# Kernel tuning notes

Hardware: AMD Instinct MI355X
Metric: run time of the kernel (lower is better)

The kernel has to match this reference:

```python
import jax, jax.numpy as jnp
import numpy as np

EPS_NORM = 1e-5   # instance-norm epsilon (NormalizeLayer over spatial axes)
EPS_VAR = 1e-9    # floor used before sqrt, as in the original


def _instance_norm(x):
    # normalize over spatial axes (1,2), per batch & channel
    mean = jnp.mean(x, axis=(1, 2), keepdims=True)
    var = jnp.var(x, axis=(1, 2), keepdims=True)
    return (x - mean) * jax.lax.rsqrt(var + EPS_NORM)


def _aat(content, style, comb_c, comb_s):
    # content/style: (B,H,W,C); comb_*: (B,H,W,Cc)
    B, H, W, C = content.shape
    N = H * W
    norm_content = _instance_norm(content)
    q = _instance_norm(comb_c).reshape(B, N, -1)   # (B,N,Cc)
    k = _instance_norm(comb_s).reshape(B, N, -1)   # (B,N,Cc)
    v = style.reshape(B, N, C)                     # (B,N,C)
    scores = jnp.einsum('bnc,bmc->bnm', q, k)      # Q_T @ K
    A = jax.nn.softmax(scores, axis=-1)            # (B,N,N)
    M = jnp.einsum('bnm,bmc->bnc', A, v)           # weighted mean
    S2 = jnp.einsum('bnm,bmc->bnc', A, v * v) - M * M  # weighted variance
    S = jnp.sqrt(jnp.maximum(jax.nn.relu(S2), EPS_VAR))
    S = S.reshape(B, H, W, C)
    M = M.reshape(B, H, W, C)
    return S * norm_content + M


def _feature_loss(cs, c, s, cc, sc):
    aat = _aat(c, s, cc, sc)
    return jnp.mean(jnp.square(cs - aat))


def setup_inputs() -> dict:
    key = jax.random.key(0)
    shapes = {
        'cs2': (4, 64, 64, 256), 'c2': (4, 64, 64, 256), 's2': (4, 64, 64, 256),
        'cc2': (4, 64, 64, 448), 'sc2': (4, 64, 64, 448),
        'cs3': (4, 32, 32, 512), 'c3': (4, 32, 32, 512), 's3': (4, 32, 32, 512),
        'cc3': (4, 32, 32, 960), 'sc3': (4, 32, 32, 960),
        'cs4': (4, 16, 16, 512), 'c4': (4, 16, 16, 512), 's4': (4, 16, 16, 512),
        'cc4': (4, 16, 16, 1472), 'sc4': (4, 16, 16, 1472),
    }
    keys = jax.random.split(key, len(shapes))
    return {name: jax.random.normal(k, shp, dtype=jnp.float32)
            for k, (name, shp) in zip(keys, shapes.items())}


def reference(cs2, c2, s2, cc2, sc2, cs3, c3, s3, cc3, sc3, cs4, c4, s4, cc4, sc4):
    loss = _feature_loss(cs2, c2, s2, cc2, sc2)
    loss = loss + _feature_loss(cs3, c3, s3, cc3, sc3)
    loss = loss + _feature_loss(cs4, c4, s4, cc4, sc4)
    return loss
```

## Files before the change

kernel.cpp:

```cpp
#include <hip/hip_runtime.h>
#include <math.h>

#define EPS_NORM 1e-5f
#define EPS_VAR  1e-9f
#define LOG2E    1.4426950408889634f

typedef unsigned short ushort_t;
typedef __attribute__((ext_vector_type(4))) float f32x4;
typedef _Float16 half8 __attribute__((ext_vector_type(8)));

#define MFMAH(a, b, c) __builtin_amdgcn_mfma_f32_16x16x32_f16((a), (b), (c), 0, 0, 0)

#define GLD16(gp, lp) __builtin_amdgcn_global_load_lds(                          \
    (const __attribute__((address_space(1))) unsigned int*)(gp),                 \
    (__attribute__((address_space(3))) unsigned int*)(lp), 16, 0, 0)

__device__ inline ushort_t f16_bits(float x) {
    _Float16 h = (_Float16)x;
    ushort_t u;
    __builtin_memcpy(&u, &h, 2);
    return u;
}
__device__ inline half8 ldh(const ushort_t* p) {
    half8 h;
    __builtin_memcpy(&h, p, 16);
    return h;
}
__device__ inline uint4 pack8(const ushort_t* s) {
    uint4 r;
    r.x = (unsigned)s[0] | ((unsigned)s[1] << 16);
    r.y = (unsigned)s[2] | ((unsigned)s[3] << 16);
    r.z = (unsigned)s[4] | ((unsigned)s[5] << 16);
    r.w = (unsigned)s[6] | ((unsigned)s[7] << 16);
    return r;
}

struct StatJobs {
    const float* x[9];
    float* sm[9];
    float* sq[9];
    int N[9], Cn[9], chG[9], nG[9], base[9];
};
__global__ void __launch_bounds__(256) stat_partial_all(StatJobs J)
{
    int bx = blockIdx.x;
    int j = 0;
#pragma unroll
    for (int k = 1; k < 9; ++k) if (bx >= J.base[k]) j = k;
    bx -= J.base[j];
    const int N = J.N[j], Cn = J.Cn[j], chG = J.chG[j], nG = J.nG[j];
    int b  = bx / (chG * nG);
    int r  = bx % (chG * nG);
    int cg = r / nG;
    int ng = r % nG;
    int ch = cg * 256 + threadIdx.x;
    if (ch >= Cn) return;
    int n0 = ng * 256;
    int n1 = min(n0 + 256, N);
    const float* p = J.x[j] + (long)(b * N) * Cn + ch;
    float s = 0.f, ss = 0.f;
    for (int n = n0; n < n1; ++n) {
        float v = p[(long)n * Cn];
        s += v;
        ss = fmaf(v, v, ss);
    }
    atomicAdd(&J.sm[j][b * Cn + ch], s);
    atomicAdd(&J.sq[j][b * Cn + ch], ss);
}

struct FinJobs {
    float* sm[9];
    float* sq[9];
    int base[9];
    float invN[9];
    int total;
};
__global__ void __launch_bounds__(256) stat_finalize_all(FinJobs J)
{
    int i = blockIdx.x * 256 + threadIdx.x;
    if (i >= J.total) return;
    int j = 0;
#pragma unroll
    for (int k = 1; k < 9; ++k) if (i >= J.base[k]) j = k;
    int e = i - J.base[j];
    float m = J.sm[j][e] * J.invN[j];
    float v = J.sq[j][e] * J.invN[j] - m * m;
    J.sm[j][e] = m;
    J.sq[j][e] = rsqrtf(v + EPS_NORM);
}

struct PrepJobs {
    const float* qx[3]; const float* qm[3]; const float* qr[3]; ushort_t* qh[3];
    const float* kx[3]; const float* km[3]; const float* kr[3]; ushort_t* kh[3];
    const float* vx[3]; ushort_t* vt[3];
    int N[3], Cc[3], C[3], nbase[3];
};
__global__ void __launch_bounds__(256) prep_all(PrepJobs J)
{
    __shared__ __align__(16) ushort_t tbuf[64 * 72];
    int bx = blockIdx.x;
    int j = 0;
#pragma unroll
    for (int k = 1; k < 3; ++k) if (bx >= J.nbase[k]) j = k;
    bx -= J.nbase[j];
    const int N = J.N[j], Cc = J.Cc[j];
    const int normBlocks = 2 * N;
    if (bx < normBlocks) {
        const int wave = threadIdx.x >> 6, lane = threadIdx.x & 63;
        int rr = bx * 4 + wave;
        const int BN = 4 * N;
        const bool isQ = rr < BN;
        int bn = isQ ? rr : rr - BN;
        const float* x    = isQ ? J.qx[j] : J.kx[j];
        const float* mean = isQ ? J.qm[j] : J.km[j];
        const float* rstd = isQ ? J.qr[j] : J.kr[j];
        ushort_t* out     = isQ ? J.qh[j] : J.kh[j];
        const float scl   = isQ ? LOG2E : 1.0f;
        int b = bn / N;
        long base = (long)bn * Cc;
        const float* mb = mean + b * Cc;
        const float* rb = rstd + b * Cc;
        for (int c8 = lane; c8 * 8 < Cc; c8 += 64) {
            int ch = c8 * 8;
            float4 a0 = *(const float4*)(x + base + ch);
            float4 a1 = *(const float4*)(x + base + ch + 4);
            float4 m0 = *(const float4*)(mb + ch);
            float4 m1 = *(const float4*)(mb + ch + 4);
            float4 r0 = *(const float4*)(rb + ch);
            float4 r1 = *(const float4*)(rb + ch + 4);
            ushort_t h8[8];
            h8[0] = f16_bits((a0.x - m0.x) * r0.x * scl);
            h8[1] = f16_bits((a0.y - m0.y) * r0.y * scl);
            h8[2] = f16_bits((a0.z - m0.z) * r0.z * scl);
            h8[3] = f16_bits((a0.w - m0.w) * r0.w * scl);
            h8[4] = f16_bits((a1.x - m1.x) * r1.x * scl);
            h8[5] = f16_bits((a1.y - m1.y) * r1.y * scl);
            h8[6] = f16_bits((a1.z - m1.z) * r1.z * scl);
            h8[7] = f16_bits((a1.w - m1.w) * r1.w * scl);
            *(uint4*)(out + base + ch) = pack8(h8);
        }
    } else {
        int bid2 = bx - normBlocks;
        const int C = J.C[j];
        const int cT = C >> 6, nT = N >> 6;
        int b   = bid2 / (cT * nT);
        int rem = bid2 % (cT * nT);
        int ch0 = (rem / nT) << 6;
        int n0  = (rem % nT) << 6;
        const int lane = threadIdx.x & 63, wv = threadIdx.x >> 6;
        const float* vb_ = J.vx[j] + (long)b * N * C + ch0 + lane;
#pragma unroll
        for (int jj = 0; jj < 2; ++jj) {
            int nl = wv * 16 + jj * 8;
            ushort_t h8[8];
#pragma unroll
            for (int i = 0; i < 8; ++i)
                h8[i] = f16_bits(vb_[(long)(n0 + nl + i) * C]);
            *(uint4*)&tbuf[lane * 72 + nl] = pack8(h8);
        }
        __syncthreads();
        {
            const int chl = threadIdx.x >> 2;
            const int nq  = (threadIdx.x & 3) * 16;
            ushort_t* op = J.vt[j] + ((long)b * C + ch0 + chl) * N + n0 + nq;
            *(uint4*)op       = *(const uint4*)&tbuf[chl * 72 + nq];
            *(uint4*)(op + 8) = *(const uint4*)&tbuf[chl * 72 + nq + 8];
        }
    }
}

__device__ inline void stage64_async(const ushort_t* __restrict__ g, long rowBase,
                                     int gstride, int col0, ushort_t* slab, int tid)
{
    const int l  = tid & 63, w = tid >> 6;
    const int rs = l >> 3;
    const int cg = (l & 7) ^ rs;
#pragma unroll
    for (int i = 0; i < 2; ++i) {
        const int r = w * 16 + i * 8 + rs;
        const ushort_t* gp = g + (rowBase + r) * (long)gstride + col0 + (cg << 3);
        ushort_t* lp = slab + (w * 16 + i * 8) * 64 + l * 8;
        GLD16(gp, lp);
    }
}
template<int BROWS>
__device__ inline void stageQ_async(const ushort_t* __restrict__ g, long rowBase,
                                    int gstride, int col0, ushort_t* slab, int tid)
{
    if (tid < BROWS * 8) {
        const int l  = tid & 63, w = tid >> 6;
        const int rs = l >> 3;
        const int cg = (l & 7) ^ rs;
        const int r  = w * 8 + rs;
        const ushort_t* gp = g + (rowBase + r) * (long)gstride + col0 + (cg << 3);
        ushort_t* lp = slab + w * 8 * 64 + l * 8;
        GLD16(gp, lp);
    }
}
__device__ inline half8 ldsw(const ushort_t* slab, int row, int soff)
{
    const int gr = (soff >> 3) ^ (row & 7);
    return ldh(slab + row * 64 + (gr << 3));
}

__global__ void __launch_bounds__(256, 2) flash_pipe(
    const ushort_t* __restrict__ Qh, const ushort_t* __restrict__ Kh,
    const ushort_t* __restrict__ Vth,
    float* __restrict__ Pmo, float* __restrict__ Plo,
    float* __restrict__ PMo, float* __restrict__ PSo)
{
    constexpr int Cc = 448, C = 256, N = 4096, SPLIT = 2;
    constexpr int NKT  = (N / 64) / SPLIT;
    constexpr long VCHO = 64L * N;
    constexpr long KADV = 64L * Cc;

    __shared__ __align__(16) ushort_t smem[4 * 8192 + 4 * 1152];
    const int tid  = threadIdx.x;
    const int lane = tid & 63;
    const int w    = tid >> 6;
    const int l15  = lane & 15;
    const int quad = lane >> 4;
// ... 408 lines not shown
        half8 pf1 = ldh(Pw + l15 * 72 + 32 + quad * 8);

#pragma unroll
        for (int g = 0; g < VCW; g += G) {
            __syncthreads();
#pragma unroll
            for (int s = 0; s < 4; ++s) {
                const int h = s / G, j = s % G;
                stage64_async(Vth, (long)b * C + (h * VCW + g + j) * 64, N, kt * 64,
                              smem + s * 4096, tid);
            }
            __syncthreads();
#pragma unroll
            for (int ks = 0; ks < 2; ++ks) {
                half8 pf = ks ? pf1 : pf0;
#pragma unroll
                for (int j = 0; j < G; ++j)
#pragma unroll
                    for (int ct = 0; ct < 4; ++ct) {
                        half8 vh = ldsw(smem + (ch2 * G + j) * 4096,
                                        ct * 16 + l15, ks * 32 + quad * 8);
                        half8 uh = vh * vh;
                        const int ci = (g + j) * 4 + ct;
                        Mac[ci] = MFMAH(pf, vh, Mac[ci]);
                        Sac[ci] = MFMAH(pf, uh, Sac[ci]);
                    }
            }
        }
    }

#pragma unroll
    for (int off = 1; off <= 8; off <<= 1)
#pragma unroll
        for (int r = 0; r < 4; ++r) l_l[r] += __shfl_xor(l_l[r], off, 64);

    if (ch2 == 0 && l15 == 0) {
#pragma unroll
        for (int r = 0; r < 4; ++r) {
            Pmo[po * 16 + quad * 4 + r] = m_r[r];
            Plo[po * 16 + quad * 4 + r] = l_l[r];
        }
    }
    const int chb = ch2 * (C / CSPLIT);
#pragma unroll
    for (int ct = 0; ct < CTCW; ++ct)
#pragma unroll
        for (int r = 0; r < 4; ++r) {
            long idx = (po * 16 + quad * 4 + r) * C + chb + ct * 16 + l15;
            PMo[idx] = Mac[ct][r];
            PSo[idx] = Sac[ct][r];
        }
}

template<int Cc, int C, int N, int CSPLIT, bool QREG, int SPLIT, int SLABS, int KGRP>
__global__ void __launch_bounds__(256, 2) flash_mfma(
    const ushort_t* __restrict__ Qh, const ushort_t* __restrict__ Kh,
    const ushort_t* __restrict__ Vth,
    float* __restrict__ Pmo, float* __restrict__ Plo,
    float* __restrict__ PMo, float* __restrict__ PSo)
{
    __shared__ __align__(16) ushort_t smem[35328];
    flash_body<Cc, C, N, CSPLIT, QREG, SPLIT, SLABS, KGRP>(
        Qh, Kh, Vth, Pmo, Plo, PMo, PSo, smem, (int)blockIdx.x);
}

__global__ void __launch_bounds__(256, 2) flash34(
    const ushort_t* __restrict__ Qh3, const ushort_t* __restrict__ Kh3,
    const ushort_t* __restrict__ Vth3,
    float* __restrict__ Pm3, float* __restrict__ Pl3,
    float* __restrict__ PM3, float* __restrict__ PS3,
    const ushort_t* __restrict__ Qh4, const ushort_t* __restrict__ Kh4,
    const ushort_t* __restrict__ Vth4,
    float* __restrict__ Pm4, float* __restrict__ Pl4,
    float* __restrict__ PM4, float* __restrict__ PS4, int G3)
{
    __shared__ __align__(16) ushort_t smem[35328];
    if ((int)blockIdx.x < G3)
        flash_body<960, 512, 1024, 2, false, 4, 5, 5>(
            Qh3, Kh3, Vth3, Pm3, Pl3, PM3, PS3, smem, (int)blockIdx.x);
    else
        flash_body<1472, 512, 256, 4, false, 4, 6, 6>(
            Qh4, Kh4, Vth4, Pm4, Pl4, PM4, PS4, smem, (int)blockIdx.x - G3);
}

template<int C, int SPLIT>
__device__ __forceinline__ void combine_body(
    const float* __restrict__ Pm, const float* __restrict__ Pl,
    const float* __restrict__ PM, const float* __restrict__ PS,
    const float* __restrict__ CT, const float* __restrict__ CS,
    const float* __restrict__ cmean, const float* __restrict__ crstd,
    float* __restrict__ loss, int N, int pi, float* shm)
{
    constexpr int CL4 = C / 4;
    float (*wS)[16] = (float(*)[16])shm;
    float* invL = shm + SPLIT * 16;
    float* red  = invL + 16;
    const int nb = N / 16;
    const int b  = pi / nb;
    const long g0 = (long)b * N + (long)(pi % nb) * 16;
    const int tid = threadIdx.x;

    if (tid < 16) {
        float m = -1e30f;
#pragma unroll
        for (int s = 0; s < SPLIT; ++s)
            m = fmaxf(m, Pm[((long)pi * SPLIT + s) * 16 + tid]);
        float L = 0.f;
#pragma unroll
        for (int s = 0; s < SPLIT; ++s) {
            float e = exp2f(Pm[((long)pi * SPLIT + s) * 16 + tid] - m);
            wS[s][tid] = e;
            L = fmaf(e, Pl[((long)pi * SPLIT + s) * 16 + tid], L);
        }
        invL[tid] = 1.f / L;
    }
    __syncthreads();

    float acc = 0.f;
    for (int v = tid; v < 4 * C; v += 256) {
        const int r  = v / CL4;
        const int c0 = (v - r * CL4) * 4;
        const long q0 = (((long)pi * SPLIT) * 16 + r) * C + c0;
        float4 Ms = {0.f, 0.f, 0.f, 0.f}, Ss = {0.f, 0.f, 0.f, 0.f};
#pragma unroll
        for (int s = 0; s < SPLIT; ++s) {
            const float ws_ = wS[s][r];
            const float4 pm = *(const float4*)&PM[q0 + (long)s * 16 * C];
            const float4 ps = *(const float4*)&PS[q0 + (long)s * 16 * C];
            Ms.x = fmaf(ws_, pm.x, Ms.x); Ms.y = fmaf(ws_, pm.y, Ms.y);
            Ms.z = fmaf(ws_, pm.z, Ms.z); Ms.w = fmaf(ws_, pm.w, Ms.w);
            Ss.x = fmaf(ws_, ps.x, Ss.x); Ss.y = fmaf(ws_, ps.y, Ss.y);
            Ss.z = fmaf(ws_, ps.z, Ss.z); Ss.w = fmaf(ws_, ps.w, Ss.w);
        }
        const float iL = invL[r];
        const float4 ctv = *(const float4*)&CT[(g0 + r) * C + c0];
        const float4 csv = *(const float4*)&CS[(g0 + r) * C + c0];
        const float4 cmv = *(const float4*)&cmean[b * C + c0];
        const float4 crv = *(const float4*)&crstd[b * C + c0];
#pragma unroll
        for (int e = 0; e < 4; ++e) {
            const float Msx = (&Ms.x)[e] * iL;
            const float S2  = (&Ss.x)[e] * iL - Msx * Msx;
            const float Sx  = sqrtf(fmaxf(S2, EPS_VAR));
            const float nc  = ((&ctv.x)[e] - (&cmv.x)[e]) * (&crv.x)[e];
            const float d   = (&csv.x)[e] - (Sx * nc + Msx);
            acc = fmaf(d, d, acc);
        }
    }
#pragma unroll
    for (int off = 1; off <= 32; off <<= 1) acc += __shfl_xor(acc, off, 64);
    if ((tid & 63) == 0) red[tid >> 6] = acc;
    __syncthreads();
    if (tid == 0) atomicAdd(loss, red[0] + red[1] + red[2] + red[3]);
}

template<int C, int SPLIT>
__global__ void __launch_bounds__(256) combine_aat(
    const float* __restrict__ Pm, const float* __restrict__ Pl,
    const float* __restrict__ PM, const float* __restrict__ PS,
    const float* __restrict__ CT, const float* __restrict__ CS,
    const float* __restrict__ cmean, const float* __restrict__ crstd,
    float* __restrict__ loss, int N)
{
    __shared__ float shm[SPLIT * 16 + 20];
    combine_body<C, SPLIT>(Pm, Pl, PM, PS, CT, CS, cmean, crstd, loss, N,
                           (int)blockIdx.x, shm);
}

__global__ void __launch_bounds__(256) combine34(
    const float* __restrict__ Pm3, const float* __restrict__ Pl3,
    const float* __restrict__ PM3, const float* __restrict__ PS3,
    const float* __restrict__ CT3, const float* __restrict__ CS3,
    const float* __restrict__ cm3, const float* __restrict__ cr3,
    float* __restrict__ l3, int N3,
    const float* __restrict__ Pm4, const float* __restrict__ Pl4,
    const float* __restrict__ PM4, const float* __restrict__ PS4,
    const float* __restrict__ CT4, const float* __restrict__ CS4,
    const float* __restrict__ cm4, const float* __restrict__ cr4,
    float* __restrict__ l4, int N4, int G3)
{
    __shared__ float shm[4 * 16 + 20];
    if ((int)blockIdx.x < G3)
        combine_body<512, 4>(Pm3, Pl3, PM3, PS3, CT3, CS3, cm3, cr3, l3, N3,
                             (int)blockIdx.x, shm);
    else
        combine_body<512, 4>(Pm4, Pl4, PM4, PS4, CT4, CS4, cm4, cr4, l4, N4,
                             (int)blockIdx.x - G3, shm);
}

template<int CCL, int CL, int NQ>
__global__ void __launch_bounds__(256) flash_aat(
    const float* __restrict__ Q, const float* __restrict__ K, const float* __restrict__ V,
    const float* __restrict__ CT, const float* __restrict__ CS,
    const float* __restrict__ qmean, const float* __restrict__ qrstd,
    const float* __restrict__ kmean, const float* __restrict__ krstd,
    const float* __restrict__ cmean, const float* __restrict__ crstd,
    float* __restrict__ loss, int N)
{
    constexpr int CC   = CCL * 64;
    constexpr int C    = CL * 64;
    constexpr int ROWS = 4 * NQ;
    const int lane = threadIdx.x & 63;
    const int wave = threadIdx.x >> 6;
    const int rowBlocks = N / ROWS;
    const int b  = blockIdx.x / rowBlocks;
    const int rb = blockIdx.x % rowBlocks;
    const int i0 = rb * ROWS + wave * NQ;

    float kmu[CCL], krs[CCL];
#pragma unroll
    for (int t = 0; t < CCL; ++t) {
        int ch = lane + 64 * t;
        kmu[t] = kmean[b * CC + ch];
        krs[t] = krstd[b * CC + ch];
    }
    float q[NQ][CCL];
#pragma unroll
    for (int qi = 0; qi < NQ; ++qi) {
        long base = (long)(b * N + i0 + qi) * CC;
#pragma unroll
        for (int t = 0; t < CCL; ++t) {
            int ch = lane + 64 * t;
            q[qi][t] = (Q[base + ch] - qmean[b * CC + ch]) * qrstd[b * CC + ch];
        }
    }
    float mval[NQ], lsum[NQ];
    float Macc[NQ][CL], Sacc[NQ][CL];
#pragma unroll
    for (int qi = 0; qi < NQ; ++qi) {
        mval[qi] = -1e30f; lsum[qi] = 0.f;
#pragma unroll
        for (int t = 0; t < CL; ++t) { Macc[qi][t] = 0.f; Sacc[qi][t] = 0.f; }
    }
    for (int j = 0; j < N; ++j) {
        long kb = (long)(b * N + j) * CC;
        float dot[NQ];
#pragma unroll
        for (int qi = 0; qi < NQ; ++qi) dot[qi] = 0.f;
#pragma unroll
        for (int t = 0; t < CCL; ++t) {
// ... 57 lines not shown
}

extern "C" void kernel_launch(void* const* d_in, const int* in_sizes, int n_in,
                              void* d_out, int out_size, void* d_ws, size_t ws_size,
                              hipStream_t stream)
{
    const float* cs2 = (const float*)d_in[0];
    const float* c2  = (const float*)d_in[1];
    const float* s2v = (const float*)d_in[2];
    const float* cc2 = (const float*)d_in[3];
    const float* sc2 = (const float*)d_in[4];
    const float* cs3 = (const float*)d_in[5];
    const float* c3  = (const float*)d_in[6];
    const float* s3v = (const float*)d_in[7];
    const float* cc3 = (const float*)d_in[8];
    const float* sc3 = (const float*)d_in[9];
    const float* cs4 = (const float*)d_in[10];
    const float* c4  = (const float*)d_in[11];
    const float* s4v = (const float*)d_in[12];
    const float* cc4 = (const float*)d_in[13];
    const float* sc4 = (const float*)d_in[14];

    const int B = 4;
    float* ws = (float*)d_ws;
    size_t fo = 0;
    auto allocF = [&](size_t n) { float* p = ws + fo; fo += n; return p; };

    float* lossp = allocF(4);
    float* c2m = allocF(B * 256);  float* c2r = allocF(B * 256);
    float* q2m = allocF(B * 448);  float* q2r = allocF(B * 448);
    float* k2m = allocF(B * 448);  float* k2r = allocF(B * 448);
    float* c3m = allocF(B * 512);  float* c3r = allocF(B * 512);
    float* q3m = allocF(B * 960);  float* q3r = allocF(B * 960);
    float* k3m = allocF(B * 960);  float* k3r = allocF(B * 960);
    float* c4m = allocF(B * 512);  float* c4r = allocF(B * 512);
    float* q4m = allocF(B * 1472); float* q4r = allocF(B * 1472);
    float* k4m = allocF(B * 1472); float* k4r = allocF(B * 1472);
    size_t zeroBytes = fo * sizeof(float);

    float* Pm = allocF(32768);
    float* Pl = allocF(32768);
    float* PM = allocF(8388608);
    float* PS = allocF(8388608);

    size_t arenaOff = ((fo * 4 + 15) & ~(size_t)15) / 2;
    ushort_t* arena = (ushort_t*)d_ws + arenaOff;
    const size_t arenaShorts = 18874400;
    size_t need = arenaOff * 2 + arenaShorts * 2;
    const bool fast = (ws_size >= need);

    hipMemsetAsync(d_ws, 0, zeroBytes, stream);

    {
        StatJobs SJ; FinJobs FJ;
        const float* xs[9] = {c2, cc2, sc2, c3, cc3, sc3, c4, cc4, sc4};
        float* sms[9] = {c2m, q2m, k2m, c3m, q3m, k3m, c4m, q4m, k4m};
        float* sqs[9] = {c2r, q2r, k2r, c3r, q3r, k3r, c4r, q4r, k4r};
        const int Ns[9]  = {4096, 4096, 4096, 1024, 1024, 1024, 256, 256, 256};
        const int Cns[9] = {256, 448, 448, 512, 960, 960, 512, 1472, 1472};
        int pb = 0, fb = 0;
        for (int j = 0; j < 9; ++j) {
            int chG = (Cns[j] + 255) / 256;
            int nG  = (Ns[j] + 255) / 256;
            SJ.x[j] = xs[j]; SJ.sm[j] = sms[j]; SJ.sq[j] = sqs[j];
            SJ.N[j] = Ns[j]; SJ.Cn[j] = Cns[j]; SJ.chG[j] = chG; SJ.nG[j] = nG;
            SJ.base[j] = pb;
            pb += B * chG * nG;
            FJ.sm[j] = sms[j]; FJ.sq[j] = sqs[j]; FJ.base[j] = fb;
            FJ.invN[j] = 1.0f / (float)Ns[j];
            fb += B * Cns[j];
        }
        FJ.total = fb;
        hipLaunchKernelGGL(stat_partial_all, dim3(pb), dim3(256), 0, stream, SJ);
        hipLaunchKernelGGL(stat_finalize_all, dim3((fb + 255) / 256), dim3(256), 0, stream, FJ);
    }

    if (fast) {
        auto arenaFor = [&](size_t& o, size_t n) {
            ushort_t* p = arena + o; o += (n + 7) & ~(size_t)7; return p;
        };
        size_t o2 = 0;
        ushort_t* qh2 = arenaFor(o2, (size_t)B*4096*448);
        ushort_t* kh2 = arenaFor(o2, (size_t)B*4096*448);
        ushort_t* vh2 = arenaFor(o2, (size_t)B*4096*256);
        size_t o3 = 0;
        ushort_t* qh3 = arenaFor(o3, (size_t)B*1024*960);
        ushort_t* kh3 = arenaFor(o3, (size_t)B*1024*960);
        ushort_t* vh3 = arenaFor(o3, (size_t)B*1024*512);
        size_t o4 = 0;
        ushort_t* qh4 = arenaFor(o4, (size_t)B*256*1472);
        ushort_t* kh4 = arenaFor(o4, (size_t)B*256*1472);
        ushort_t* vh4 = arenaFor(o4, (size_t)B*256*512);

        const int vt2 = (256/64)*(4096/64)*B;
        const int vt3 = (512/64)*(1024/64)*B;
        const int vt4 = (512/64)*(256/64)*B;

        size_t totShorts = o2 + o3 + o4;
        bool prepFused = (ws_size >= arenaOff * 2 + totShorts * 2);

        const size_t PS4N = (size_t)256 * 16 * 512;
        size_t tailByte = (((arenaOff + totShorts) * 2) + 255) & ~(size_t)255;
        bool fused34 = prepFused && (ws_size >= tailByte + 2 * PS4N * 4);
        float* PM4 = nullptr; float* PS4 = nullptr;
        if (fused34) {
            PM4 = (float*)((char*)d_ws + tailByte);
            PS4 = PM4 + PS4N;
        }

        if (prepFused) {
            qh3 = arena + o2;        kh3 = qh3 + (((size_t)B*1024*960 + 7) & ~(size_t)7);
            vh3 = kh3 + (((size_t)B*1024*960 + 7) & ~(size_t)7);
            qh4 = arena + o2 + o3;   kh4 = qh4 + (((size_t)B*256*1472 + 7) & ~(size_t)7);
            vh4 = kh4 + (((size_t)B*256*1472 + 7) & ~(size_t)7);

            PrepJobs PJ;
            PJ.qx[0]=cc2; PJ.qm[0]=q2m; PJ.qr[0]=q2r; PJ.qh[0]=qh2;
            PJ.kx[0]=sc2; PJ.km[0]=k2m; PJ.kr[0]=k2r; PJ.kh[0]=kh2;
            PJ.vx[0]=s2v; PJ.vt[0]=vh2; PJ.N[0]=4096; PJ.Cc[0]=448; PJ.C[0]=256;
            PJ.qx[1]=cc3; PJ.qm[1]=q3m; PJ.qr[1]=q3r; PJ.qh[1]=qh3;
            PJ.kx[1]=sc3; PJ.km[1]=k3m; PJ.kr[1]=k3r; PJ.kh[1]=kh3;
            PJ.vx[1]=s3v; PJ.vt[1]=vh3; PJ.N[1]=1024; PJ.Cc[1]=960; PJ.C[1]=512;
            PJ.qx[2]=cc4; PJ.qm[2]=q4m; PJ.qr[2]=q4r; PJ.qh[2]=qh4;
            PJ.kx[2]=sc4; PJ.km[2]=k4m; PJ.kr[2]=k4r; PJ.kh[2]=kh4;
            PJ.vx[2]=s4v; PJ.vt[2]=vh4; PJ.N[2]=256;  PJ.Cc[2]=1472; PJ.C[2]=512;
            int g0n = 2*4096 + vt2;
            int g1n = 2*1024 + vt3;
            int g2n = 2*256  + vt4;
            PJ.nbase[0] = 0; PJ.nbase[1] = g0n; PJ.nbase[2] = g0n + g1n;
            hipLaunchKernelGGL(prep_all, dim3(g0n + g1n + g2n), dim3(256), 0, stream, PJ);
        }

        {
            if (!prepFused) {
                PrepJobs PJ;
                PJ.qx[0]=cc2; PJ.qm[0]=q2m; PJ.qr[0]=q2r; PJ.qh[0]=qh2;
                PJ.kx[0]=sc2; PJ.km[0]=k2m; PJ.kr[0]=k2r; PJ.kh[0]=kh2;
                PJ.vx[0]=s2v; PJ.vt[0]=vh2; PJ.N[0]=4096; PJ.Cc[0]=448; PJ.C[0]=256;
                for (int k = 1; k < 3; ++k) { PJ.N[k]=4096; PJ.Cc[k]=448; PJ.C[k]=256;
                    PJ.qx[k]=cc2; PJ.qm[k]=q2m; PJ.qr[k]=q2r; PJ.qh[k]=qh2;
                    PJ.kx[k]=sc2; PJ.km[k]=k2m; PJ.kr[k]=k2r; PJ.kh[k]=kh2;
                    PJ.vx[k]=s2v; PJ.vt[k]=vh2; }
                int gn = 2*4096 + vt2;
                PJ.nbase[0]=0; PJ.nbase[1]=gn; PJ.nbase[2]=gn;
                hipLaunchKernelGGL(prep_all, dim3(gn), dim3(256), 0, stream, PJ);
            }
            hipLaunchKernelGGL(flash_pipe, dim3(B*(4096/64)*2), dim3(256), 0, stream,
                               qh2, kh2, vh2, Pm, Pl, PM, PS);
            hipLaunchKernelGGL((combine_aat<256, 2>), dim3(B*4096/16), dim3(256), 0, stream,
                               Pm, Pl, PM, PS, c2, cs2, c2m, c2r, &lossp[0], 4096);
        }

        if (fused34) {
            const int G3 = B*(1024/32)*4;
            const int G4 = B*(256/16)*4;
            hipLaunchKernelGGL(flash34, dim3(G3 + G4), dim3(256), 0, stream,
                               qh3, kh3, vh3, Pm, Pl, PM, PS,
                               qh4, kh4, vh4, Pm + 16384, Pl + 16384, PM4, PS4, G3);
            const int C3 = B*1024/16;
            const int C4 = B*256/16;
            hipLaunchKernelGGL(combine34, dim3(C3 + C4), dim3(256), 0, stream,
                               Pm, Pl, PM, PS, c3, cs3, c3m, c3r, &lossp[1], 1024,
                               Pm + 16384, Pl + 16384, PM4, PS4,
                               c4, cs4, c4m, c4r, &lossp[2], 256, C3);
        } else {
            {
                if (!prepFused) {
                    PrepJobs PJ;
                    PJ.qx[0]=cc3; PJ.qm[0]=q3m; PJ.qr[0]=q3r; PJ.qh[0]=qh3;
                    PJ.kx[0]=sc3; PJ.km[0]=k3m; PJ.kr[0]=k3r; PJ.kh[0]=kh3;
                    PJ.vx[0]=s3v; PJ.vt[0]=vh3; PJ.N[0]=1024; PJ.Cc[0]=960; PJ.C[0]=512;
                    for (int k = 1; k < 3; ++k) { PJ.N[k]=1024; PJ.Cc[k]=960; PJ.C[k]=512;
                        PJ.qx[k]=cc3; PJ.qm[k]=q3m; PJ.qr[k]=q3r; PJ.qh[k]=qh3;
                        PJ.kx[k]=sc3; PJ.km[k]=k3m; PJ.kr[k]=k3r; PJ.kh[k]=kh3;
                        PJ.vx[k]=s3v; PJ.vt[k]=vh3; }
                    int gn = 2*1024 + vt3;
                    PJ.nbase[0]=0; PJ.nbase[1]=gn; PJ.nbase[2]=gn;
                    hipLaunchKernelGGL(prep_all, dim3(gn), dim3(256), 0, stream, PJ);
                }
                hipLaunchKernelGGL((flash_mfma<960, 512, 1024, 2, false, 4, 5, 5>),
                                   dim3(B*(1024/32)*4), dim3(256), 0, stream,
                                   qh3, kh3, vh3, Pm, Pl, PM, PS);
                hipLaunchKernelGGL((combine_aat<512, 4>), dim3(B*1024/16), dim3(256), 0, stream,
                                   Pm, Pl, PM, PS, c3, cs3, c3m, c3r, &lossp[1], 1024);
            }
            {
                if (!prepFused) {
                    PrepJobs PJ;
                    PJ.qx[0]=cc4; PJ.qm[0]=q4m; PJ.qr[0]=q4r; PJ.qh[0]=qh4;
                    PJ.kx[0]=sc4; PJ.km[0]=k4m; PJ.kr[0]=k4r; PJ.kh[0]=kh4;
                    PJ.vx[0]=s4v; PJ.vt[0]=vh4; PJ.N[0]=256; PJ.Cc[0]=1472; PJ.C[0]=512;
                    for (int k = 1; k < 3; ++k) { PJ.N[k]=256; PJ.Cc[k]=1472; PJ.C[k]=512;
                        PJ.qx[k]=cc4; PJ.qm[k]=q4m; PJ.qr[k]=q4r; PJ.qh[k]=qh4;
                        PJ.kx[k]=sc4; PJ.km[k]=k4m; PJ.kr[k]=k4r; PJ.kh[k]=kh4;
                        PJ.vx[k]=s4v; PJ.vt[k]=vh4; }
                    int gn = 2*256 + vt4;
                    PJ.nbase[0]=0; PJ.nbase[1]=gn; PJ.nbase[2]=gn;
                    hipLaunchKernelGGL(prep_all, dim3(gn), dim3(256), 0, stream, PJ);
                }
                hipLaunchKernelGGL((flash_mfma<1472, 512, 256, 4, false, 4, 6, 6>),
                                   dim3(B*(256/16)*4), dim3(256), 0, stream,
                                   qh4, kh4, vh4, Pm, Pl, PM, PS);
                hipLaunchKernelGGL((combine_aat<512, 4>), dim3(B*256/16), dim3(256), 0, stream,
                                   Pm, Pl, PM, PS, c4, cs4, c4m, c4r, &lossp[2], 256);
            }
        }
    } else {
        hipLaunchKernelGGL((flash_aat<7, 4, 4>), dim3(B * 4096 / 16), dim3(256), 0, stream,
                           cc2, sc2, s2v, c2, cs2, q2m, q2r, k2m, k2r, c2m, c2r, &lossp[0], 4096);
        hipLaunchKernelGGL((flash_aat<15, 8, 2>), dim3(B * 1024 / 8), dim3(256), 0, stream,
                           cc3, sc3, s3v, c3, cs3, q3m, q3r, k3m, k3r, c3m, c3r, &lossp[1], 1024);
        hipLaunchKernelGGL((flash_aat<23, 8, 2>), dim3(B * 256 / 8), dim3(256), 0, stream,
                           cc4, sc4, s4v, c4, cs4, q4m, q4r, k4m, k4r, c4m, c4r, &lossp[2], 256);
    }

    hipLaunchKernelGGL(combine_loss, dim3(1), dim3(1), 0, stream,
                       lossp, (float*)d_out,
                       1.0f / (4.0f * 4096.0f * 256.0f),
                       1.0f / (4.0f * 1024.0f * 512.0f),
                       1.0f / (4.0f * 256.0f * 512.0f));
}
```

Before: 672.4 us.

## Fuse stat finalize, prep, and combine stages to cut kernel launches

Drops the separate stat-finalize kernel and folds the mean/rstd computation into the norm-prep and combine consumers. Level-2 combine now runs in the same launch as the level-3/4 prep, and the final loss reduction moves into the last combine kernel through an atomic last-block counter. It also halves the row chunk per block in the statistics pass and lowers the level-4 flash split to 2. The aim is fewer launches and serial gaps, at the cost of recomputing rsqrt per element and hardcoding shapes and grid sizes.

```diff
diff --git a/kernel.cpp b/kernel.cpp
--- a/kernel.cpp
+++ b/kernel.cpp
@@ -55,8 +55,8 @@
     int ng = r % nG;
     int ch = cg * 256 + threadIdx.x;
     if (ch >= Cn) return;
-    int n0 = ng * 256;
-    int n1 = min(n0 + 256, N);
+    int n0 = ng * 128;
+    int n1 = min(n0 + 128, N);
     const float* p = J.x[j] + (long)(b * N) * Cn + ch;
     float s = 0.f, ss = 0.f;
     for (int n = n0; n < n1; ++n) {
@@ -89,84 +89,92 @@
     J.sq[j][e] = rsqrtf(v + EPS_NORM);
 }
 
-struct PrepJobs {
-    const float* qx[3]; const float* qm[3]; const float* qr[3]; ushort_t* qh[3];
-    const float* kx[3]; const float* km[3]; const float* kr[3]; ushort_t* kh[3];
-    const float* vx[3]; ushort_t* vt[3];
-    int N[3], Cc[3], C[3], nbase[3];
-};
-__global__ void __launch_bounds__(256) prep_all(PrepJobs J)
-{
-    __shared__ __align__(16) ushort_t tbuf[64 * 72];
+__device__ __forceinline__ void norm_quad(
+    int bx, const float* __restrict__ qx, const float* __restrict__ qs,
+    const float* __restrict__ qq, const float* __restrict__ kx,
+    const float* __restrict__ ks, const float* __restrict__ kq,
+    ushort_t* __restrict__ qh, ushort_t* __restrict__ kh,
+    int N, int Cc, float invN)
+{
+    const int wave = threadIdx.x >> 6, lane = threadIdx.x & 63;
+    int rr = bx * 4 + wave;
+    const int BN = 4 * N;
+    const bool isQ = rr < BN;
+    int bn = isQ ? rr : rr - BN;
+    const float* x  = isQ ? qx : kx;
+    const float* sm = isQ ? qs : ks;
+    const float* sq = isQ ? qq : kq;
+    ushort_t* out   = isQ ? qh : kh;
+    const float scl = isQ ? LOG2E : 1.0f;
+    int b = bn / N;
+    long base = (long)bn * Cc;
+    const float* smb = sm + b * Cc;
+    const float* sqb = sq + b * Cc;
+    for (int c8 = lane; c8 * 8 < Cc; c8 += 64) {
+        int ch = c8 * 8;
+        float4 a0 = *(const float4*)(x + base + ch);
+        float4 a1 = *(const float4*)(x + base + ch + 4);
+        float4 s0 = *(const float4*)(smb + ch);
+        float4 s1 = *(const float4*)(smb + ch + 4);
+        float4 t0 = *(const float4*)(sqb + ch);
+        float4 t1 = *(const float4*)(sqb + ch + 4);
+        ushort_t h8[8];
+#pragma unroll
+        for (int e = 0; e < 4; ++e) {
+            float m = (&s0.x)[e] * invN;
+            float r = rsqrtf((&t0.x)[e] * invN - m * m + EPS_NORM);
+            h8[e] = f16_bits(((&a0.x)[e] - m) * r * scl);
+        }
+#pragma unroll
+        for (int e = 0; e < 4; ++e) {
+            float m = (&s1.x)[e] * invN;
+            float r = rsqrtf((&t1.x)[e] * invN - m * m + EPS_NORM);
+            h8[4 + e] = f16_bits(((&a1.x)[e] - m) * r * scl);
+        }
+        *(uint4*)(out + base + ch) = pack8(h8);
+    }
+}
+
+__device__ __forceinline__ void vtile(
+    int bid2, const float* __restrict__ vx, ushort_t* __restrict__ vt,
+    int N, int C, ushort_t* tbuf)
+{
+    const int cT = C >> 6, nT = N >> 6;
+    int b   = bid2 / (cT * nT);
+    int rem = bid2 % (cT * nT);
+    int ch0 = (rem / nT) << 6;
+    int n0  = (rem % nT) << 6;
+    const int lane = threadIdx.x & 63, wv = threadIdx.x >> 6;
+    const float* vb_ = vx + (long)b * N * C + ch0 + lane;
+#pragma unroll
+    for (int jj = 0; jj < 2; ++jj) {
+        int nl = wv * 16 + jj * 8;
+        ushort_t h8[8];
+#pragma unroll
+        for (int i = 0; i < 8; ++i)
+            h8[i] = f16_bits(vb_[(long)(n0 + nl + i) * C]);
+        *(uint4*)&tbuf[lane * 72 + nl] = pack8(h8);
+    }
+    __syncthreads();
+    {
+        const int chl = threadIdx.x >> 2;
+        const int nq  = (threadIdx.x & 3) * 16;
+        ushort_t* op = vt + ((long)b * C + ch0 + chl) * N + n0 + nq;
+        *(uint4*)op       = *(const uint4*)&tbuf[chl * 72 + nq];
+        *(uint4*)(op + 8) = *(const uint4*)&tbuf[chl * 72 + nq + 8];
+    }
+}
+
+__global__ void __launch_bounds__(256) prep2(
+    const float* __restrict__ qx, const float* __restrict__ qs, const float* __restrict__ qq,
+    const float* __restrict__ kx, const float* __restrict__ ks, const float* __restrict__ kq,
+    ushort_t* __restrict__ qh, ushort_t* __restrict__ kh,
+    const float* __restrict__ vx, ushort_t* __restrict__ vt)
+{
+    __shared__ __align__(16) ushort_t lbuf[4608];
     int bx = blockIdx.x;
-    int j = 0;
-#pragma unroll
-    for (int k = 1; k < 3; ++k) if (bx >= J.nbase[k]) j = k;
-    bx -= J.nbase[j];
-    const int N = J.N[j], Cc = J.Cc[j];
-    const int normBlocks = 2 * N;
-    if (bx < normBlocks) {
-        const int wave = threadIdx.x >> 6, lane = threadIdx.x & 63;
-        int rr = bx * 4 + wave;
-        const int BN = 4 * N;
-        const bool isQ = rr < BN;
-        int bn = isQ ? rr : rr - BN;
-        const float* x    = isQ ? J.qx[j] : J.kx[j];
-        const float* mean = isQ ? J.qm[j] : J.km[j];
-        const float* rstd = isQ ? J.qr[j] : J.kr[j];
-        ushort_t* out     = isQ ? J.qh[j] : J.kh[j];
-        const float scl   = isQ ? LOG2E : 1.0f;
-        int b = bn / N;
-        long base = (long)bn * Cc;
-        const float* mb = mean + b * Cc;
-        const float* rb = rstd + b * Cc;
-        for (int c8 = lane; c8 * 8 < Cc; c8 += 64) {
-            int ch = c8 * 8;
-            float4 a0 = *(const float4*)(x + base + ch);
-            float4 a1 = *(const float4*)(x + base + ch + 4);
-            float4 m0 = *(const float4*)(mb + ch);
-            float4 m1 = *(const float4*)(mb + ch + 4);
-            float4 r0 = *(const float4*)(rb + ch);
-            float4 r1 = *(const float4*)(rb + ch + 4);
-            ushort_t h8[8];
-            h8[0] = f16_bits((a0.x - m0.x) * r0.x * scl);
-            h8[1] = f16_bits((a0.y - m0.y) * r0.y * scl);
-            h8[2] = f16_bits((a0.z - m0.z) * r0.z * scl);
-            h8[3] = f16_bits((a0.w - m0.w) * r0.w * scl);
-            h8[4] = f16_bits((a1.x - m1.x) * r1.x * scl);
-            h8[5] = f16_bits((a1.y - m1.y) * r1.y * scl);
-            h8[6] = f16_bits((a1.z - m1.z) * r1.z * scl);
-            h8[7] = f16_bits((a1.w - m1.w) * r1.w * scl);
-            *(uint4*)(out + base + ch) = pack8(h8);
-        }
-    } else {
-        int bid2 = bx - normBlocks;
-        const int C = J.C[j];
-        const int cT = C >> 6, nT = N >> 6;
-        int b   = bid2 / (cT * nT);
-        int rem = bid2 % (cT * nT);
-        int ch0 = (rem / nT) << 6;
-        int n0  = (rem % nT) << 6;
-        const int lane = threadIdx.x & 63, wv = threadIdx.x >> 6;
-        const float* vb_ = J.vx[j] + (long)b * N * C + ch0 + lane;
-#pragma unroll
-        for (int jj = 0; jj < 2; ++jj) {
-            int nl = wv * 16 + jj * 8;
-            ushort_t h8[8];
-#pragma unroll
-            for (int i = 0; i < 8; ++i)
-                h8[i] = f16_bits(vb_[(long)(n0 + nl + i) * C]);
-            *(uint4*)&tbuf[lane * 72 + nl] = pack8(h8);
-        }
-        __syncthreads();
-        {
-            const int chl = threadIdx.x >> 2;
-            const int nq  = (threadIdx.x & 3) * 16;
-            ushort_t* op = J.vt[j] + ((long)b * C + ch0 + chl) * N + n0 + nq;
-            *(uint4*)op       = *(const uint4*)&tbuf[chl * 72 + nq];
-            *(uint4*)(op + 8) = *(const uint4*)&tbuf[chl * 72 + nq + 8];
-        }
-    }
+    if (bx < 8192) norm_quad(bx, qx, qs, qq, kx, ks, kq, qh, kh, 4096, 448, 1.0f / 4096.0f);
+    else           vtile(bx - 8192, vx, vt, 4096, 256, lbuf);
 }
 
 __device__ inline void stage64_async(const ushort_t* __restrict__ g, long rowBase,
@@ -681,18 +689,6 @@
         }
 }
 
-template<int Cc, int C, int N, int CSPLIT, bool QREG, int SPLIT, int SLABS, int KGRP>
-__global__ void __launch_bounds__(256, 2) flash_mfma(
-    const ushort_t* __restrict__ Qh, const ushort_t* __restrict__ Kh,
-    const ushort_t* __restrict__ Vth,
-    float* __restrict__ Pmo, float* __restrict__ Plo,
-    float* __restrict__ PMo, float* __restrict__ PSo)
-{
-    __shared__ __align__(16) ushort_t smem[35328];
-    flash_body<Cc, C, N, CSPLIT, QREG, SPLIT, SLABS, KGRP>(
-        Qh, Kh, Vth, Pmo, Plo, PMo, PSo, smem, (int)blockIdx.x);
-}
-
 __global__ void __launch_bounds__(256, 2) flash34(
     const ushort_t* __restrict__ Qh3, const ushort_t* __restrict__ Kh3,
     const ushort_t* __restrict__ Vth3,
@@ -701,15 +697,15 @@
     const ushort_t* __restrict__ Qh4, const ushort_t* __restrict__ Kh4,
     const ushort_t* __restrict__ Vth4,
     float* __restrict__ Pm4, float* __restrict__ Pl4,
-    float* __restrict__ PM4, float* __restrict__ PS4, int G3)
+    float* __restrict__ PM4, float* __restrict__ PS4)
 {
     __shared__ __align__(16) ushort_t smem[35328];
-    if ((int)blockIdx.x < G3)
+    if ((int)blockIdx.x < 512)
         flash_body<960, 512, 1024, 2, false, 4, 5, 5>(
             Qh3, Kh3, Vth3, Pm3, Pl3, PM3, PS3, smem, (int)blockIdx.x);
     else
-        flash_body<1472, 512, 256, 4, false, 4, 6, 6>(
-            Qh4, Kh4, Vth4, Pm4, Pl4, PM4, PS4, smem, (int)blockIdx.x - G3);
+        flash_body<1472, 512, 256, 4, false, 2, 6, 6>(
+            Qh4, Kh4, Vth4, Pm4, Pl4, PM4, PS4, smem, (int)blockIdx.x - 512);
 }
 
 template<int C, int SPLIT>
@@ -717,8 +713,8 @@
     const float* __restrict__ Pm, const float* __restrict__ Pl,
     const float* __restrict__ PM, const float* __restrict__ PS,
     const float* __restrict__ CT, const float* __restrict__ CS,
-    const float* __restrict__ cmean, const float* __restrict__ crstd,
-    float* __restrict__ loss, int N, int pi, float* shm)
+    const float* __restrict__ csum, const float* __restrict__ csq,
+    float invN, float* __restrict__ loss, int N, int pi, float* shm)
 {
     constexpr int CL4 = C / 4;
     float (*wS)[16] = (float(*)[16])shm;
@@ -764,14 +760,16 @@
         const float iL = invL[r];
         const float4 ctv = *(const float4*)&CT[(g0 + r) * C + c0];
         const float4 csv = *(const float4*)&CS[(g0 + r) * C + c0];
-        const float4 cmv = *(const float4*)&cmean[b * C + c0];
-        const float4 crv = *(const float4*)&crstd[b * C + c0];
+        const float4 cs4 = *(const float4*)&csum[b * C + c0];
+        const float4 cq4 = *(const float4*)&csq[b * C + c0];
 #pragma unroll
         for (int e = 0; e < 4; ++e) {
             const float Msx = (&Ms.x)[e] * iL;
             const float S2  = (&Ss.x)[e] * iL - Msx * Msx;
             const float Sx  = sqrtf(fmaxf(S2, EPS_VAR));
-            const float nc  = ((&ctv.x)[e] - (&cmv.x)[e]) * (&crv.x)[e];
+            const float cm  = (&cs4.x)[e] * invN;
+            const float cr  = rsqrtf((&cq4.x)[e] * invN - cm * cm + EPS_NORM);
+            const float nc  = ((&ctv.x)[e] - cm) * cr;
             const float d   = (&csv.x)[e] - (Sx * nc + Msx);
             acc = fmaf(d, d, acc);
         }
@@ -783,38 +781,61 @@
     if (tid == 0) atomicAdd(loss, red[0] + red[1] + red[2] + red[3]);
 }
 
-template<int C, int SPLIT>
-__global__ void __launch_bounds__(256) combine_aat(
-    const float* __restrict__ Pm, const float* __restrict__ Pl,
-    const float* __restrict__ PM, const float* __restrict__ PS,
-    const float* __restrict__ CT, const float* __restrict__ CS,
-    const float* __restrict__ cmean, const float* __restrict__ crstd,
-    float* __restrict__ loss, int N)
-{
-    __shared__ float shm[SPLIT * 16 + 20];
-    combine_body<C, SPLIT>(Pm, Pl, PM, PS, CT, CS, cmean, crstd, loss, N,
-                           (int)blockIdx.x, shm);
-}
-
-__global__ void __launch_bounds__(256) combine34(
-    const float* __restrict__ Pm3, const float* __restrict__ Pl3,
-    const float* __restrict__ PM3, const float* __restrict__ PS3,
-    const float* __restrict__ CT3, const float* __restrict__ CS3,
-    const float* __restrict__ cm3, const float* __restrict__ cr3,
-    float* __restrict__ l3, int N3,
-    const float* __restrict__ Pm4, const float* __restrict__ Pl4,
-    const float* __restrict__ PM4, const float* __restrict__ PS4,
-    const float* __restrict__ CT4, const float* __restrict__ CS4,
-    const float* __restrict__ cm4, const float* __restrict__ cr4,
-    float* __restrict__ l4, int N4, int G3)
+struct MidP {
+    const float *Pm, *Pl, *PM, *PS, *CT, *CS, *csum, *csq;
+    float* loss;
+    const float *q3x, *q3s, *q3q, *k3x, *k3s, *k3q, *v3x;
+    ushort_t *qh3, *kh3, *vt3;
+    const float *q4x, *q4s, *q4q, *k4x, *k4s, *k4q, *v4x;
+    ushort_t *qh4, *kh4, *vt4;
+};
+__global__ void __launch_bounds__(256) mid_fused(MidP P)
+{
+    __shared__ __align__(16) ushort_t lbuf[4608];
+    int bx = blockIdx.x;
+    if (bx < 1024) {
+        combine_body<256, 2>(P.Pm, P.Pl, P.PM, P.PS, P.CT, P.CS, P.csum, P.csq,
+                             1.0f / 4096.0f, P.loss, 4096, bx, (float*)lbuf);
+    } else if (bx < 3072) {
+        norm_quad(bx - 1024, P.q3x, P.q3s, P.q3q, P.k3x, P.k3s, P.k3q,
+                  P.qh3, P.kh3, 1024, 960, 1.0f / 1024.0f);
+    } else if (bx < 3584) {
+        vtile(bx - 3072, P.v3x, P.vt3, 1024, 512, lbuf);
+    } else if (bx < 4096) {
+        norm_quad(bx - 3584, P.q4x, P.q4s, P.q4q, P.k4x, P.k4s, P.k4q,
+                  P.qh4, P.kh4, 256, 1472, 1.0f / 256.0f);
+    } else {
+        vtile(bx - 4096, P.v4x, P.vt4, 256, 512, lbuf);
+    }
+}
+
+struct C34P {
+    const float *Pm3, *Pl3, *PM3, *PS3, *CT3, *CS3, *c3s, *c3q;
+    const float *Pm4, *Pl4, *PM4, *PS4, *CT4, *CS4, *c4s, *c4q;
+    float* lossp;
+    float* out;
+    float s0, s1, s2;
+};
+__global__ void __launch_bounds__(256) combine34_final(C34P P)
 {
     __shared__ float shm[4 * 16 + 20];
-    if ((int)blockIdx.x < G3)
-        combine_body<512, 4>(Pm3, Pl3, PM3, PS3, CT3, CS3, cm3, cr3, l3, N3,
-                             (int)blockIdx.x, shm);
+    int bx = blockIdx.x;
+    if (bx < 256)
+        combine_body<512, 4>(P.Pm3, P.Pl3, P.PM3, P.PS3, P.CT3, P.CS3, P.c3s, P.c3q,
+                             1.0f / 1024.0f, &P.lossp[1], 1024, bx, shm);
     else
-        combine_body<512, 4>(Pm4, Pl4, PM4, PS4, CT4, CS4, cm4, cr4, l4, N4,
-                             (int)blockIdx.x - G3, shm);
+        combine_body<512, 2>(P.Pm4, P.Pl4, P.PM4, P.PS4, P.CT4, P.CS4, P.c4s, P.c4q,
+                             1.0f / 256.0f, &P.lossp[2], 256, bx - 256, shm);
+    __threadfence();
+    if (threadIdx.x == 0) {
+        unsigned old = atomicAdd((unsigned*)&P.lossp[3], 1u);
+        if (old == 319u) {
+            float l0 = atomicAdd(&P.lossp[0], 0.0f);
+            float l1 = atomicAdd(&P.lossp[1], 0.0f);
+            float l2 = atomicAdd(&P.lossp[2], 0.0f);
+            P.out[0] = l0 * P.s0 + l1 * P.s1 + l2 * P.s2;
+        }
+    }
 }
 
 template<int CCL, int CL, int NQ>
@@ -978,171 +999,99 @@
     hipMemsetAsync(d_ws, 0, zeroBytes, stream);
 
     {
-        StatJobs SJ; FinJobs FJ;
+        StatJobs SJ;
         const float* xs[9] = {c2, cc2, sc2, c3, cc3, sc3, c4, cc4, sc4};
         float* sms[9] = {c2m, q2m, k2m, c3m, q3m, k3m, c4m, q4m, k4m};
         float* sqs[9] = {c2r, q2r, k2r, c3r, q3r, k3r, c4r, q4r, k4r};
         const int Ns[9]  = {4096, 4096, 4096, 1024, 1024, 1024, 256, 256, 256};
         const int Cns[9] = {256, 448, 448, 512, 960, 960, 512, 1472, 1472};
-        int pb = 0, fb = 0;
+        int pb = 0;
         for (int j = 0; j < 9; ++j) {
             int chG = (Cns[j] + 255) / 256;
-            int nG  = (Ns[j] + 255) / 256;
+            int nG  = (Ns[j] + 127) / 128;
             SJ.x[j] = xs[j]; SJ.sm[j] = sms[j]; SJ.sq[j] = sqs[j];
             SJ.N[j] = Ns[j]; SJ.Cn[j] = Cns[j]; SJ.chG[j] = chG; SJ.nG[j] = nG;
             SJ.base[j] = pb;
             pb += B * chG * nG;
-            FJ.sm[j] = sms[j]; FJ.sq[j] = sqs[j]; FJ.base[j] = fb;
-            FJ.invN[j] = 1.0f / (float)Ns[j];
-            fb += B * Cns[j];
-        }
-        FJ.total = fb;
+        }
         hipLaunchKernelGGL(stat_partial_all, dim3(pb), dim3(256), 0, stream, SJ);
-        hipLaunchKernelGGL(stat_finalize_all, dim3((fb + 255) / 256), dim3(256), 0, stream, FJ);
     }
 
     if (fast) {
-        auto arenaFor = [&](size_t& o, size_t n) {
-            ushort_t* p = arena + o; o += (n + 7) & ~(size_t)7; return p;
-        };
-        size_t o2 = 0;
-        ushort_t* qh2 = arenaFor(o2, (size_t)B*4096*448);
-        ushort_t* kh2 = arenaFor(o2, (size_t)B*4096*448);
-        ushort_t* vh2 = arenaFor(o2, (size_t)B*4096*256);
-        size_t o3 = 0;
-        ushort_t* qh3 = arenaFor(o3, (size_t)B*1024*960);
-        ushort_t* kh3 = arenaFor(o3, (size_t)B*1024*960);
-        ushort_t* vh3 = arenaFor(o3, (size_t)B*1024*512);
-        size_t o4 = 0;
-        ushort_t* qh4 = arenaFor(o4, (size_t)B*256*1472);
-        ushort_t* kh4 = arenaFor(o4, (size_t)B*256*1472);
-        ushort_t* vh4 = arenaFor(o4, (size_t)B*256*512);
-
-        const int vt2 = (256/64)*(4096/64)*B;
-        const int vt3 = (512/64)*(1024/64)*B;
-        const int vt4 = (512/64)*(256/64)*B;
-
-        size_t totShorts = o2 + o3 + o4;
-        bool prepFused = (ws_size >= arenaOff * 2 + totShorts * 2);
-
-        const size_t PS4N = (size_t)256 * 16 * 512;
-        size_t tailByte = (((arenaOff + totShorts) * 2) + 255) & ~(size_t)255;
-        bool fused34 = prepFused && (ws_size >= tailByte + 2 * PS4N * 4);
-        float* PM4 = nullptr; float* PS4 = nullptr;
-        if (fused34) {
-            PM4 = (float*)((char*)d_ws + tailByte);
-            PS4 = PM4 + PS4N;
-        }
-
-        if (prepFused) {
-            qh3 = arena + o2;        kh3 = qh3 + (((size_t)B*1024*960 + 7) & ~(size_t)7);
-            vh3 = kh3 + (((size_t)B*1024*960 + 7) & ~(size_t)7);
-            qh4 = arena + o2 + o3;   kh4 = qh4 + (((size_t)B*256*1472 + 7) & ~(size_t)7);
-            vh4 = kh4 + (((size_t)B*256*1472 + 7) & ~(size_t)7);
-
-            PrepJobs PJ;
-            PJ.qx[0]=cc2; PJ.qm[0]=q2m; PJ.qr[0]=q2r; PJ.qh[0]=qh2;
-            PJ.kx[0]=sc2; PJ.km[0]=k2m; PJ.kr[0]=k2r; PJ.kh[0]=kh2;
-            PJ.vx[0]=s2v; PJ.vt[0]=vh2; PJ.N[0]=4096; PJ.Cc[0]=448; PJ.C[0]=256;
-            PJ.qx[1]=cc3; PJ.qm[1]=q3m; PJ.qr[1]=q3r; PJ.qh[1]=qh3;
-            PJ.kx[1]=sc3; PJ.km[1]=k3m; PJ.kr[1]=k3r; PJ.kh[1]=kh3;
-            PJ.vx[1]=s3v; PJ.vt[1]=vh3; PJ.N[1]=1024; PJ.Cc[1]=960; PJ.C[1]=512;
-            PJ.qx[2]=cc4; PJ.qm[2]=q4m; PJ.qr[2]=q4r; PJ.qh[2]=qh4;
-            PJ.kx[2]=sc4; PJ.km[2]=k4m; PJ.kr[2]=k4r; PJ.kh[2]=kh4;
-            PJ.vx[2]=s4v; PJ.vt[2]=vh4; PJ.N[2]=256;  PJ.Cc[2]=1472; PJ.C[2]=512;
-            int g0n = 2*4096 + vt2;
-            int g1n = 2*1024 + vt3;
-            int g2n = 2*256  + vt4;
-            PJ.nbase[0] = 0; PJ.nbase[1] = g0n; PJ.nbase[2] = g0n + g1n;
-            hipLaunchKernelGGL(prep_all, dim3(g0n + g1n + g2n), dim3(256), 0, stream, PJ);
-        }
-
+        ushort_t* qh2 = arena;
+        ushort_t* kh2 = qh2 + (size_t)B * 4096 * 448;
+        ushort_t* vh2 = kh2 + (size_t)B * 4096 * 448;
+        ushort_t* qh3 = arena;
+        ushort_t* kh3 = qh3 + (size_t)B * 1024 * 960;
+        ushort_t* vh3 = kh3 + (size_t)B * 1024 * 960;
+        ushort_t* qh4 = vh3 + (size_t)B * 1024 * 512;
+        ushort_t* kh4 = qh4 + (size_t)B * 256 * 1472;
+        ushort_t* vh4 = kh4 + (size_t)B * 256 * 1472;
+        size_t o34 = (size_t)B * 1024 * 960 * 2 + (size_t)B * 1024 * 512
+                   + (size_t)B * 256 * 1472 * 2 + (size_t)B * 256 * 512;
+        float* PM4 = (float*)(arena + o34);
+        float* PS4 = PM4 + 1048576;
+        float* Pm4 = Pm + 16384;
+        float* Pl4 = Pl + 16384;
+
+        hipLaunchKernelGGL(prep2, dim3(8192 + 1024), dim3(256), 0, stream,
+                           cc2, q2m, q2r, sc2, k2m, k2r, qh2, kh2, s2v, vh2);
+        hipLaunchKernelGGL(flash_pipe, dim3(512), dim3(256), 0, stream,
+                           qh2, kh2, vh2, Pm, Pl, PM, PS);
         {
-            if (!prepFused) {
-                PrepJobs PJ;
-                PJ.qx[0]=cc2; PJ.qm[0]=q2m; PJ.qr[0]=q2r; PJ.qh[0]=qh2;
-                PJ.kx[0]=sc2; PJ.km[0]=k2m; PJ.kr[0]=k2r; PJ.kh[0]=kh2;
-                PJ.vx[0]=s2v; PJ.vt[0]=vh2; PJ.N[0]=4096; PJ.Cc[0]=448; PJ.C[0]=256;
-                for (int k = 1; k < 3; ++k) { PJ.N[k]=4096; PJ.Cc[k]=448; PJ.C[k]=256;
-                    PJ.qx[k]=cc2; PJ.qm[k]=q2m; PJ.qr[k]=q2r; PJ.qh[k]=qh2;
-                    PJ.kx[k]=sc2; PJ.km[k]=k2m; PJ.kr[k]=k2r; PJ.kh[k]=kh2;
-                    PJ.vx[k]=s2v; PJ.vt[k]=vh2; }
-                int gn = 2*4096 + vt2;
-                PJ.nbase[0]=0; PJ.nbase[1]=gn; PJ.nbase[2]=gn;
-                hipLaunchKernelGGL(prep_all, dim3(gn), dim3(256), 0, stream, PJ);
+            MidP MP;
+            MP.Pm = Pm; MP.Pl = Pl; MP.PM = PM; MP.PS = PS;
+            MP.CT = c2; MP.CS = cs2; MP.csum = c2m; MP.csq = c2r;
+            MP.loss = &lossp[0];
+            MP.q3x = cc3; MP.q3s = q3m; MP.q3q = q3r;
+            MP.k3x = sc3; MP.k3s = k3m; MP.k3q = k3r; MP.v3x = s3v;
+            MP.qh3 = qh3; MP.kh3 = kh3; MP.vt3 = vh3;
+            MP.q4x = cc4; MP.q4s = q4m; MP.q4q = q4r;
+            MP.k4x = sc4; MP.k4s = k4m; MP.k4q = k4r; MP.v4x = s4v;
+            MP.qh4 = qh4; MP.kh4 = kh4; MP.vt4 = vh4;
+            hipLaunchKernelGGL(mid_fused, dim3(4224), dim3(256), 0, stream, MP);
+        }
+        hipLaunchKernelGGL(flash34, dim3(512 + 128), dim3(256), 0, stream,
+                           qh3, kh3, vh3, Pm, Pl, PM, PS,
+                           qh4, kh4, vh4, Pm4, Pl4, PM4, PS4);
+        {
+            C34P CP;
+            CP.Pm3 = Pm; CP.Pl3 = Pl; CP.PM3 = PM; CP.PS3 = PS;
+            CP.CT3 = c3; CP.CS3 = cs3; CP.c3s = c3m; CP.c3q = c3r;
+            CP.Pm4 = Pm4; CP.Pl4 = Pl4; CP.PM4 = PM4; CP.PS4 = PS4;
+            CP.CT4 = c4; CP.CS4 = cs4; CP.c4s = c4m; CP.c4q = c4r;
+            CP.lossp = lossp; CP.out = (float*)d_out;
+            CP.s0 = 1.0f / (4.0f * 4096.0f * 256.0f);
+            CP.s1 = 1.0f / (4.0f * 1024.0f * 512.0f);
+            CP.s2 = 1.0f / (4.0f * 256.0f * 512.0f);
+            hipLaunchKernelGGL(combine34_final, dim3(256 + 64), dim3(256), 0, stream, CP);
+        }
+    } else {
+        {
+            FinJobs FJ;
+            float* sms[9] = {c2m, q2m, k2m, c3m, q3m, k3m, c4m, q4m, k4m};
+            float* sqs[9] = {c2r, q2r, k2r, c3r, q3r, k3r, c4r, q4r, k4r};
+            const int Ns[9]  = {4096, 4096, 4096, 1024, 1024, 1024, 256, 256, 256};
+            const int Cns[9] = {256, 448, 448, 512, 960, 960, 512, 1472, 1472};
+            int fb = 0;
+            for (int j = 0; j < 9; ++j) {
+                FJ.sm[j] = sms[j]; FJ.sq[j] = sqs[j]; FJ.base[j] = fb;
+                FJ.invN[j] = 1.0f / (float)Ns[j];
+                fb += B * Cns[j];
             }
-            hipLaunchKernelGGL(flash_pipe, dim3(B*(4096/64)*2), dim3(256), 0, stream,
-                               qh2, kh2, vh2, Pm, Pl, PM, PS);
-            hipLaunchKernelGGL((combine_aat<256, 2>), dim3(B*4096/16), dim3(256), 0, stream,
-                               Pm, Pl, PM, PS, c2, cs2, c2m, c2r, &lossp[0], 4096);
-        }
-
-        if (fused34) {
-            const int G3 = B*(1024/32)*4;
-            const int G4 = B*(256/16)*4;
-            hipLaunchKernelGGL(flash34, dim3(G3 + G4), dim3(256), 0, stream,
-                               qh3, kh3, vh3, Pm, Pl, PM, PS,
-                               qh4, kh4, vh4, Pm + 16384, Pl + 16384, PM4, PS4, G3);
-            const int C3 = B*1024/16;
-            const int C4 = B*256/16;
-            hipLaunchKernelGGL(combine34, dim3(C3 + C4), dim3(256), 0, stream,
-                               Pm, Pl, PM, PS, c3, cs3, c3m, c3r, &lossp[1], 1024,
-                               Pm + 16384, Pl + 16384, PM4, PS4,
-                               c4, cs4, c4m, c4r, &lossp[2], 256, C3);
-        } else {
-            {
-                if (!prepFused) {
-                    PrepJobs PJ;
-                    PJ.qx[0]=cc3; PJ.qm[0]=q3m; PJ.qr[0]=q3r; PJ.qh[0]=qh3;
-                    PJ.kx[0]=sc3; PJ.km[0]=k3m; PJ.kr[0]=k3r; PJ.kh[0]=kh3;
-                    PJ.vx[0]=s3v; PJ.vt[0]=vh3; PJ.N[0]=1024; PJ.Cc[0]=960; PJ.C[0]=512;
-                    for (int k = 1; k < 3; ++k) { PJ.N[k]=1024; PJ.Cc[k]=960; PJ.C[k]=512;
-                        PJ.qx[k]=cc3; PJ.qm[k]=q3m; PJ.qr[k]=q3r; PJ.qh[k]=qh3;
-                        PJ.kx[k]=sc3; PJ.km[k]=k3m; PJ.kr[k]=k3r; PJ.kh[k]=kh3;
-                        PJ.vx[k]=s3v; PJ.vt[k]=vh3; }
-                    int gn = 2*1024 + vt3;
-                    PJ.nbase[0]=0; PJ.nbase[1]=gn; PJ.nbase[2]=gn;
-                    hipLaunchKernelGGL(prep_all, dim3(gn), dim3(256), 0, stream, PJ);
-                }
-                hipLaunchKernelGGL((flash_mfma<960, 512, 1024, 2, false, 4, 5, 5>),
-                                   dim3(B*(1024/32)*4), dim3(256), 0, stream,
-                                   qh3, kh3, vh3, Pm, Pl, PM, PS);
-                hipLaunchKernelGGL((combine_aat<512, 4>), dim3(B*1024/16), dim3(256), 0, stream,
-                                   Pm, Pl, PM, PS, c3, cs3, c3m, c3r, &lossp[1], 1024);
-            }
-            {
-                if (!prepFused) {
-                    PrepJobs PJ;
-                    PJ.qx[0]=cc4; PJ.qm[0]=q4m; PJ.qr[0]=q4r; PJ.qh[0]=qh4;
-                    PJ.kx[0]=sc4; PJ.km[0]=k4m; PJ.kr[0]=k4r; PJ.kh[0]=kh4;
-                    PJ.vx[0]=s4v; PJ.vt[0]=vh4; PJ.N[0]=256; PJ.Cc[0]=1472; PJ.C[0]=512;
-                    for (int k = 1; k < 3; ++k) { PJ.N[k]=256; PJ.Cc[k]=1472; PJ.C[k]=512;
-                        PJ.qx[k]=cc4; PJ.qm[k]=q4m; PJ.qr[k]=q4r; PJ.qh[k]=qh4;
-                        PJ.kx[k]=sc4; PJ.km[k]=k4m; PJ.kr[k]=k4r; PJ.kh[k]=kh4;
-                        PJ.vx[k]=s4v; PJ.vt[k]=vh4; }
-                    int gn = 2*256 + vt4;
-                    PJ.nbase[0]=0; PJ.nbase[1]=gn; PJ.nbase[2]=gn;
-                    hipLaunchKernelGGL(prep_all, dim3(gn), dim3(256), 0, stream, PJ);
-                }
-                hipLaunchKernelGGL((flash_mfma<1472, 512, 256, 4, false, 4, 6, 6>),
-                                   dim3(B*(256/16)*4), dim3(256), 0, stream,
-                                   qh4, kh4, vh4, Pm, Pl, PM, PS);
-                hipLaunchKernelGGL((combine_aat<512, 4>), dim3(B*256/16), dim3(256), 0, stream,
-                                   Pm, Pl, PM, PS, c4, cs4, c4m, c4r, &lossp[2], 256);
-            }
-        }
-    } else {
+            FJ.total = fb;
+            hipLaunchKernelGGL(stat_finalize_all, dim3((fb + 255) / 256), dim3(256), 0, stream, FJ);
+        }
         hipLaunchKernelGGL((flash_aat<7, 4, 4>), dim3(B * 4096 / 16), dim3(256), 0, stream,
                            cc2, sc2, s2v, c2, cs2, q2m, q2r, k2m, k2r, c2m, c2r, &lossp[0], 4096);
         hipLaunchKernelGGL((flash_aat<15, 8, 2>), dim3(B * 1024 / 8), dim3(256), 0, stream,
                            cc3, sc3, s3v, c3, cs3, q3m, q3r, k3m, k3r, c3m, c3r, &lossp[1], 1024);
         hipLaunchKernelGGL((flash_aat<23, 8, 2>), dim3(B * 256 / 8), dim3(256), 0, stream,
                            cc4, sc4, s4v, c4, cs4, q4m, q4r, k4m, k4r, c4m, c4r, &lossp[2], 256);
-    }
-
-    hipLaunchKernelGGL(combine_loss, dim3(1), dim3(1), 0, stream,
-                       lossp, (float*)d_out,
-                       1.0f / (4.0f * 4096.0f * 256.0f),
-                       1.0f / (4.0f * 1024.0f * 512.0f),
-                       1.0f / (4.0f * 256.0f * 512.0f));
-}
+        hipLaunchKernelGGL(combine_loss, dim3(1), dim3(1), 0, stream,
+                           lossp, (float*)d_out,
+                           1.0f / (4.0f * 4096.0f * 256.0f),
+                           1.0f / (4.0f * 1024.0f * 512.0f),
+                           1.0f / (4.0f * 256.0f * 512.0f));
+    }
+}
```

New measurement: 650.3 us. -3.3%, faster.
